# Kernel tuning notes

Hardware: AMD Instinct MI355X
Metric: run time of the kernel (lower is better)

The kernel has to match this reference:

```python
import jax, jax.numpy as jnp
import numpy as np

B, S, IN_F, OUT_F = 4, 2048, 4096, 4096
ALPHA = 0.01

def setup_inputs() -> dict:
    key = jax.random.key(0)
    k1, k2 = jax.random.split(key, 2)
    # int8-valued activations and weights (stored as int32 per harness dtype)
    x = jax.random.randint(k1, (B, S, IN_F), -127, 127, dtype=jnp.int32)
    weight = jax.random.randint(k2, (IN_F, OUT_F), -127, 127, dtype=jnp.int32)
    bias = jnp.zeros((1, OUT_F), dtype=jnp.float16)
    alpha = jnp.full((1,), ALPHA, dtype=jnp.float32)
    return {"x": x, "weight": weight, "bias": bias, "alpha": alpha}

def reference(x, weight, bias, alpha):
    # Faithful to forward's default (non-hybrid) path:
    # y = F.linear(x.float(), weight.t().float(), bias.float()) * alpha
    # F.linear(x, W^T) == x @ W, with W shape (in_features, out_features).
    x_shape = x.shape
    xf = x.reshape(-1, x_shape[-1]).astype(jnp.float32)          # [B*S, in]
    wf = weight.astype(jnp.float32)                               # [in, out]
    y = (xf @ wf + bias.astype(jnp.float32)) * alpha              # [B*S, out]
    return y.reshape(*x_shape[:-1], -1)                           # [B, S, out]
```

## Files before the change

### kernel.cpp

```cpp
#include <hip/hip_runtime.h>
#include <hip/hip_fp16.h>

using i32x4  = __attribute__((ext_vector_type(4)))  int;
using i32x16 = __attribute__((ext_vector_type(16))) int;

static constexpr int M  = 4 * 2048;
static constexpr int N  = 4096;
static constexpr int K  = 4096;
static constexpr int BM = 128, BN = 128, BK = 64;
static constexpr int NT = K / BK;
static constexpr int TILE = BM * BK;

static constexpr int PX_BLOCKS = (int)((size_t)M * K / 16 / 256);
static constexpr int PW_BLOCKS = (int)((size_t)N * K / 16 / 256);

__device__ __forceinline__ unsigned pack4(i32x4 v) {
  return (unsigned)((v.x & 255) | ((v.y & 255) << 8) | ((v.z & 255) << 16) | (v.w << 24));
}

__global__ __launch_bounds__(256) void pack_kernel(const int* __restrict__ x,
                                                   const int* __restrict__ w,
                                                   unsigned char* __restrict__ wa,
                                                   unsigned char* __restrict__ wb) {
  if (blockIdx.x < PX_BLOCKS) {
    unsigned g = blockIdx.x * 256 + threadIdx.x;
    unsigned tile = g >> 9, gt = g & 511;
    unsigned kg = gt >> 7, row = gt & 127;
    unsigned br = tile >> 6, kt = tile & 63;
    const int* src = x + ((size_t)(br * 128 + row) * K + kt * 64 + kg * 16);
    i32x4 v0 = *(const i32x4*)(src + 0);
    i32x4 v1 = *(const i32x4*)(src + 4);
    i32x4 v2 = *(const i32x4*)(src + 8);
    i32x4 v3 = *(const i32x4*)(src + 12);
    i32x4 d;
    d.x = (int)pack4(v0); d.y = (int)pack4(v1); d.z = (int)pack4(v2); d.w = (int)pack4(v3);
    *(i32x4*)(wa + (size_t)g * 16) = d;
  } else {
    unsigned g = (blockIdx.x - PX_BLOCKS) * 256 + threadIdx.x;
    unsigned tile = g >> 9, gt = g & 511;
    unsigned kg = gt >> 7, col = gt & 127;
    unsigned bn = tile >> 6, kt = tile & 63;
    unsigned n  = bn * 128 + col;
    unsigned k0 = kt * 64 + kg * 16;
    const int* src = w + (size_t)k0 * N + n;
    i32x4 d;
#pragma unroll
    for (int j = 0; j < 4; ++j) {
      int b0 = src[(size_t)(j * 4 + 0) * N];
      int b1 = src[(size_t)(j * 4 + 1) * N];
      int b2 = src[(size_t)(j * 4 + 2) * N];
      int b3 = src[(size_t)(j * 4 + 3) * N];
      d[j] = (b0 & 255) | ((b1 & 255) << 8) | ((b2 & 255) << 16) | (b3 << 24);
    }
    *(i32x4*)(wb + (size_t)g * 16) = d;
  }
}


__global__ __launch_bounds__(256) void gemm_i8(const unsigned char* __restrict__ wa,
                                               const unsigned char* __restrict__ wb,
                                               const __half* __restrict__ bias,
                                               const float* __restrict__ alphaP,
                                               float* __restrict__ out) {
  __shared__ __align__(16) unsigned char As[2][TILE];
  __shared__ __align__(16) unsigned char Bs[2][TILE];

  const int tid  = threadIdx.x;
  const int lane = tid & 63;
  const int w    = tid >> 6;
  const int wr   = w >> 1, wc = w & 1;
  const int l31  = lane & 31;
  const int kgl  = lane >> 5;

  const int bc = blockIdx.x;
  const int br = blockIdx.y;

  const unsigned char* ga = wa + (size_t)br * NT * TILE;
  const unsigned char* gb = wb + (size_t)bc * NT * TILE;

  const int arow = wr * 64 + l31;
  const int bcol = wc * 64 + l31;

  i32x4 p0, p1, p2, p3;
  i32x4 q0, q1, q2, q3;

#define GLOAD_P(T) do {                                              \
    const i32x4* ap = (const i32x4*)(ga + (size_t)(T) * TILE);       \
    const i32x4* bp = (const i32x4*)(gb + (size_t)(T) * TILE);       \
    p0 = ap[tid]; p1 = ap[tid + 256];                                \
    p2 = bp[tid]; p3 = bp[tid + 256];                                \
  } while (0)

#define GLOAD_Q(T) do {                                              \
    const i32x4* ap = (const i32x4*)(ga + (size_t)(T) * TILE);       \
    const i32x4* bp = (const i32x4*)(gb + (size_t)(T) * TILE);       \
    q0 = ap[tid]; q1 = ap[tid + 256];                                \
    q2 = bp[tid]; q3 = bp[tid + 256];                                \
  } while (0)

#define SWRITE_P(BUF) do {                                           \
    i32x4* aw = (i32x4*)&As[BUF][0];                                 \
    i32x4* bw = (i32x4*)&Bs[BUF][0];                                 \
    aw[tid] = p0; aw[tid + 256] = p1;                                \
    bw[tid] = p2; bw[tid + 256] = p3;                                \
  } while (0)

#define SWRITE_Q(BUF) do {                                           \
    i32x4* aw = (i32x4*)&As[BUF][0];                                 \
    i32x4* bw = (i32x4*)&Bs[BUF][0];                                 \
    aw[tid] = q0; aw[tid + 256] = q1;                                \
    bw[tid] = q2; bw[tid + 256] = q3;                                \
  } while (0)

  i32x16 acc[2][2] = {};

#define COMPUTE(BUF) do {                                                      \
    const unsigned char* Ab = &As[BUF][0] + kgl * 2048;                        \
    const unsigned char* Bb = &Bs[BUF][0] + kgl * 2048;                        \
    _Pragma("unroll")                                                          \
    for (int kc = 0; kc < 2; ++kc) {                                           \
      const unsigned char* Ap = Ab + kc * 4096;                                \
      const unsigned char* Bp = Bb + kc * 4096;                                \
      i32x4 a0 = *(const i32x4*)(Ap + (arow +  0) * 16);                       \
      i32x4 a1 = *(const i32x4*)(Ap + (arow + 32) * 16);                       \
      i32x4 b0 = *(const i32x4*)(Bp + (bcol +  0) * 16);                       \
      i32x4 b1 = *(const i32x4*)(Bp + (bcol + 32) * 16);                       \
      acc[0][0] = __builtin_amdgcn_mfma_i32_32x32x32_i8(a0, b0, acc[0][0], 0, 0, 0); \
      acc[0][1] = __builtin_amdgcn_mfma_i32_32x32x32_i8(a0, b1, acc[0][1], 0, 0, 0); \
      acc[1][0] = __builtin_amdgcn_mfma_i32_32x32x32_i8(a1, b0, acc[1][0], 0, 0, 0); \
      acc[1][1] = __builtin_amdgcn_mfma_i32_32x32x32_i8(a1, b1, acc[1][1], 0, 0, 0); \
    }                                                                          \
  } while (0)

  GLOAD_P(0);
  SWRITE_P(0);
  GLOAD_Q(1);
  __syncthreads();

  for (int t = 0; t < NT; t += 2) {
    if (t + 2 < NT) GLOAD_P(t + 2);
    COMPUTE(0);
    __builtin_amdgcn_sched_barrier(0);
    if (t + 1 < NT) SWRITE_Q(1);
    __syncthreads();

    if (t + 3 < NT) GLOAD_Q(t + 3);
    COMPUTE(1);
    __builtin_amdgcn_sched_barrier(0);
    if (t + 2 < NT) SWRITE_P(0);
    __syncthreads();
  }

  const float alpha = *alphaP;
  const int row0 = br * 128 + wr * 64 + 4 * kgl;
  const int col0 = bc * 128 + wc * 64 + l31;
#pragma unroll
  for (int ni = 0; ni < 2; ++ni) {
    const int col = col0 + ni * 32;
    const float bf = __half2float(bias[col]);
#pragma unroll
    for (int mi = 0; mi < 2; ++mi) {
#pragma unroll
      for (int r = 0; r < 16; ++r) {
        const int row = row0 + mi * 32 + (r & 3) + 8 * (r >> 2);
        out[(size_t)row * N + col] = ((float)acc[mi][ni][r] + bf) * alpha;
      }
    }
  }
#undef COMPUTE
#undef GLOAD_P
#undef GLOAD_Q
#undef SWRITE_P
#undef SWRITE_Q
}

extern "C" void kernel_launch(void* const* d_in, const int* in_sizes, int n_in,
                              void* d_out, int out_size, void* d_ws, size_t ws_size,
                              hipStream_t stream) {
  const int*    x     = (const int*)d_in[0];
  const int*    wgt   = (const int*)d_in[1];
  const __half* bias  = (const __half*)d_in[2];
  const float*  alpha = (const float*)d_in[3];
  float*        out   = (float*)d_out;

  unsigned char* wa = (unsigned char*)d_ws;
  unsigned char* wb = wa + (size_t)M * K;

  pack_kernel<<<PX_BLOCKS + PW_BLOCKS, 256, 0, stream>>>(x, wgt, wa, wb);

  dim3 grid(N / BN, M / BM);
  gemm_i8<<<grid, 256, 0, stream>>>(wa, wb, bias, alpha, out);
}
```

Before: 227.3 us.

## Load B fragments directly from global into registers, bypassing LDS

```diff
diff --git a/kernel.cpp b/kernel.cpp
--- a/kernel.cpp
+++ b/kernel.cpp
@@ -63,7 +63,6 @@
                                                const float* __restrict__ alphaP,
                                                float* __restrict__ out) {
   __shared__ __align__(16) unsigned char As[2][TILE];
-  __shared__ __align__(16) unsigned char Bs[2][TILE];
 
   const int tid  = threadIdx.x;
   const int lane = tid & 63;
@@ -81,71 +80,71 @@
   const int arow = wr * 64 + l31;
   const int bcol = wc * 64 + l31;
 
-  i32x4 p0, p1, p2, p3;
-  i32x4 q0, q1, q2, q3;
+  i32x4 p0, p1, q0, q1;
+  i32x4 b[2][2][2];
 
-#define GLOAD_P(T) do {                                              \
+#define GLOADA_P(T) do {                                             \
     const i32x4* ap = (const i32x4*)(ga + (size_t)(T) * TILE);       \
-    const i32x4* bp = (const i32x4*)(gb + (size_t)(T) * TILE);       \
     p0 = ap[tid]; p1 = ap[tid + 256];                                \
-    p2 = bp[tid]; p3 = bp[tid + 256];                                \
   } while (0)
 
-#define GLOAD_Q(T) do {                                              \
+#define GLOADA_Q(T) do {                                             \
     const i32x4* ap = (const i32x4*)(ga + (size_t)(T) * TILE);       \
-    const i32x4* bp = (const i32x4*)(gb + (size_t)(T) * TILE);       \
     q0 = ap[tid]; q1 = ap[tid + 256];                                \
-    q2 = bp[tid]; q3 = bp[tid + 256];                                \
   } while (0)
 
 #define SWRITE_P(BUF) do {                                           \
     i32x4* aw = (i32x4*)&As[BUF][0];                                 \
-    i32x4* bw = (i32x4*)&Bs[BUF][0];                                 \
     aw[tid] = p0; aw[tid + 256] = p1;                                \
-    bw[tid] = p2; bw[tid + 256] = p3;                                \
   } while (0)
 
 #define SWRITE_Q(BUF) do {                                           \
     i32x4* aw = (i32x4*)&As[BUF][0];                                 \
-    i32x4* bw = (i32x4*)&Bs[BUF][0];                                 \
     aw[tid] = q0; aw[tid + 256] = q1;                                \
-    bw[tid] = q2; bw[tid + 256] = q3;                                \
+  } while (0)
+
+#define BLOAD(PAR, T) do {                                           \
+    const unsigned char* bt = gb + (size_t)(T) * TILE;               \
+    b[PAR][0][0] = *(const i32x4*)(bt + (kgl    ) * 2048 + (bcol +  0) * 16); \
+    b[PAR][0][1] = *(const i32x4*)(bt + (kgl    ) * 2048 + (bcol + 32) * 16); \
+    b[PAR][1][0] = *(const i32x4*)(bt + (kgl + 2) * 2048 + (bcol +  0) * 16); \
+    b[PAR][1][1] = *(const i32x4*)(bt + (kgl + 2) * 2048 + (bcol + 32) * 16); \
   } while (0)
 
   i32x16 acc[2][2] = {};
 
-#define COMPUTE(BUF) do {                                                      \
+#define COMPUTE(BUF, PAR) do {                                                 \
     const unsigned char* Ab = &As[BUF][0] + kgl * 2048;                        \
-    const unsigned char* Bb = &Bs[BUF][0] + kgl * 2048;                        \
     _Pragma("unroll")                                                          \
     for (int kc = 0; kc < 2; ++kc) {                                           \
       const unsigned char* Ap = Ab + kc * 4096;                                \
-      const unsigned char* Bp = Bb + kc * 4096;                                \
       i32x4 a0 = *(const i32x4*)(Ap + (arow +  0) * 16);                       \
       i32x4 a1 = *(const i32x4*)(Ap + (arow + 32) * 16);                       \
-      i32x4 b0 = *(const i32x4*)(Bp + (bcol +  0) * 16);                       \
-      i32x4 b1 = *(const i32x4*)(Bp + (bcol + 32) * 16);                       \
-      acc[0][0] = __builtin_amdgcn_mfma_i32_32x32x32_i8(a0, b0, acc[0][0], 0, 0, 0); \
-      acc[0][1] = __builtin_amdgcn_mfma_i32_32x32x32_i8(a0, b1, acc[0][1], 0, 0, 0); \
-      acc[1][0] = __builtin_amdgcn_mfma_i32_32x32x32_i8(a1, b0, acc[1][0], 0, 0, 0); \
-      acc[1][1] = __builtin_amdgcn_mfma_i32_32x32x32_i8(a1, b1, acc[1][1], 0, 0, 0); \
+      acc[0][0] = __builtin_amdgcn_mfma_i32_32x32x32_i8(a0, b[PAR][kc][0], acc[0][0], 0, 0, 0); \
+      acc[0][1] = __builtin_amdgcn_mfma_i32_32x32x32_i8(a0, b[PAR][kc][1], acc[0][1], 0, 0, 0); \
+      acc[1][0] = __builtin_amdgcn_mfma_i32_32x32x32_i8(a1, b[PAR][kc][0], acc[1][0], 0, 0, 0); \
+      acc[1][1] = __builtin_amdgcn_mfma_i32_32x32x32_i8(a1, b[PAR][kc][1], acc[1][1], 0, 0, 0); \
     }                                                                          \
   } while (0)
 
-  GLOAD_P(0);
+  GLOADA_P(0);
+  BLOAD(0, 0);
   SWRITE_P(0);
-  GLOAD_Q(1);
+  GLOADA_Q(1);
+  BLOAD(1, 1);
   __syncthreads();
 
   for (int t = 0; t < NT; t += 2) {
-    if (t + 2 < NT) GLOAD_P(t + 2);
-    COMPUTE(0);
+    if (t + 2 < NT) GLOADA_P(t + 2);
+    COMPUTE(0, 0);
+    if (t + 2 < NT) BLOAD(0, t + 2);
     __builtin_amdgcn_sched_barrier(0);
     if (t + 1 < NT) SWRITE_Q(1);
     __syncthreads();
 
-    if (t + 3 < NT) GLOAD_Q(t + 3);
-    COMPUTE(1);
+    if (t + 3 < NT) GLOADA_Q(t + 3);
+    COMPUTE(1, 1);
+    if (t + 3 < NT) BLOAD(1, t + 3);
     __builtin_amdgcn_sched_barrier(0);
     if (t + 2 < NT) SWRITE_P(0);
     __syncthreads();
@@ -168,10 +167,11 @@
     }
   }
 #undef COMPUTE
-#undef GLOAD_P
-#undef GLOAD_Q
+#undef GLOADA_P
+#undef GLOADA_Q
 #undef SWRITE_P
 #undef SWRITE_Q
+#undef BLOAD
 }
 
 extern "C" void kernel_launch(void* const* d_in, const int* in_sizes, int n_in,
```

New measurement: 224.8 us. No clear change (-1.1%).
